# Optimization experiments

Measured on AMD Instinct MI355X. Metric: run time of the kernel, lower is better.

The kernel has to match this reference:

```python
import jax, jax.numpy as jnp
import numpy as np

OUT_FEATURES = 4096
IN_FEATURES = 4096
SCALE_EPS = 1e-5


def setup_inputs() -> dict:
    key = jax.random.key(0)
    k1, k2, k3 = jax.random.split(key, 3)
    x = jax.random.normal(k1, (8192, IN_FEATURES), dtype=jnp.float32)
    # packed int4 weights: two signed nibbles per byte-equivalent int
    weight_packed = jax.random.randint(k2, (OUT_FEATURES, IN_FEATURES // 2), 0, 256, dtype=jnp.int32)
    weight_scale = jax.random.uniform(k3, (OUT_FEATURES,), dtype=jnp.float32) * 0.01 + 1e-4
    return {"x": x, "weight_packed": weight_packed, "weight_scale": weight_scale}


def _unpack_int4(weight_packed):
    # low nibble first, then high nibble, sign-extended from 4 bits
    low = weight_packed & 15
    high = (weight_packed >> 4) & 15
    low = jnp.where(low > 7, low - 16, low)
    high = jnp.where(high > 7, high - 16, high)
    # interleave -> [out_features, in_features]
    w_q = jnp.stack([low, high], axis=-1).reshape(weight_packed.shape[0], -1)
    return w_q


def reference(x, weight_packed, weight_scale):
    # per-row activation quantization to int4 range [-8, 7]
    x_max = jnp.max(jnp.abs(x), axis=-1, keepdims=True)
    x_scale = jnp.maximum(x_max / 7.0, SCALE_EPS)          # [tokens, 1]
    x_q = jnp.clip(jnp.round(x / x_scale), -8.0, 7.0)      # float carrier of int4 values

    w_q = _unpack_int4(weight_packed).astype(jnp.float32)  # [out, in]

    out = jnp.einsum('ti,oi->to', x_q, w_q)                # [tokens, out]
    out = out * (x_scale * weight_scale[None, :])
    return out.astype(x.dtype)
```

## Files before the change

### kernel.cpp

```cpp
#include <hip/hip_runtime.h>

#define SCALE_EPS 1e-5f

typedef int v4i __attribute__((ext_vector_type(4)));

static __device__ __forceinline__ void gll16(const void* g, void* l) {
  __builtin_amdgcn_global_load_lds(
      (const __attribute__((address_space(1))) unsigned int*)g,
      (__attribute__((address_space(3))) unsigned int*)l,
      16, 0, 0);
}

__global__ __launch_bounds__(256) void unpack_w(const int* __restrict__ wp,
                                                char* __restrict__ wq) {
  const int kc = blockIdx.x;
  const int nt = blockIdx.y;
  const int tid = threadIdx.x;
  char* tile = wq + ((size_t)nt * 64 + kc) * 8192;
  const int n0 = nt * 128;
#pragma unroll
  for (int j = 0; j < 4; ++j) {
    int u = j * 256 + tid;
    int r = u >> 3;
    int p = u & 7;
    const v4i* src = (const v4i*)((const char*)wp + (size_t)(n0 + r) * 8192 + kc * 128 + p * 16);
    v4i v = *src;
    unsigned int b[8];
#pragma unroll
    for (int q = 0; q < 4; ++q) {
      int lo = ((v[q] & 15) ^ 8) - 8;
      int hi = (((v[q] >> 4) & 15) ^ 8) - 8;
      b[q * 2]     = (unsigned int)(lo & 255);
      b[q * 2 + 1] = (unsigned int)(hi & 255);
    }
    unsigned int w0 = b[0] | (b[1] << 8) | (b[2] << 16) | (b[3] << 24);
    unsigned int w1 = b[4] | (b[5] << 8) | (b[6] << 16) | (b[7] << 24);
    *(uint2*)(tile + (r >> 4) * 1024 + (p >> 1) * 256 + (r & 15) * 16 + (p & 1) * 8) =
        make_uint2(w0, w1);
  }
}

__global__ __launch_bounds__(256) void quant_x(const float* __restrict__ x,
                                               char* __restrict__ xq,
                                               float* __restrict__ xs) {
  __shared__ float lmax[4][4];
  const int tid = threadIdx.x;
  const int w = tid >> 6;
  const int l = tid & 63;
  const int t0 = blockIdx.x * 4;
  const int row = l >> 4;
  const int t = t0 + row;
  const int sub = l & 15;

  const float* base = x + (size_t)t * 4096 + w * 1024 + sub * 4;
  float4 vals[16];
  float m = 0.0f;
#pragma unroll
  for (int s = 0; s < 16; ++s) {
    vals[s] = *(const float4*)(base + s * 64);
    m = fmaxf(m, fmaxf(fmaxf(fabsf(vals[s].x), fabsf(vals[s].y)),
                       fmaxf(fabsf(vals[s].z), fabsf(vals[s].w))));
  }
#pragma unroll
  for (int d = 1; d < 16; d <<= 1) m = fmaxf(m, __shfl_xor(m, d, 64));
  if (sub == 0) lmax[w][row] = m;
  __syncthreads();
  float rm = fmaxf(fmaxf(lmax[0][row], lmax[1][row]),
                   fmaxf(lmax[2][row], lmax[3][row]));
  float scale = fmaxf(rm / 7.0f, SCALE_EPS);
  if (w == 0 && sub == 0) xs[t] = scale;

  const int mt = t0 >> 7;
  const int f = (t0 & 127) >> 4;
  const int r16 = t & 15;
  const int cc = sub >> 2;
  const int b4 = (sub & 3) * 4;

#pragma unroll
  for (int s = 0; s < 16; ++s) {
    float4 v = vals[s];
    int q0 = (int)fminf(fmaxf(rintf(v.x / scale), -8.0f), 7.0f);
    int q1 = (int)fminf(fmaxf(rintf(v.y / scale), -8.0f), 7.0f);
    int q2 = (int)fminf(fmaxf(rintf(v.z / scale), -8.0f), 7.0f);
    int q3 = (int)fminf(fmaxf(rintf(v.w / scale), -8.0f), 7.0f);
    unsigned int wd = (unsigned int)(q0 & 255) | ((unsigned int)(q1 & 255) << 8) |
                      ((unsigned int)(q2 & 255) << 16) | ((unsigned int)(q3 & 255) << 24);
    *(unsigned int*)(xq + ((size_t)mt * 64 + w * 16 + s) * 8192 +
                     f * 1024 + cc * 256 + r16 * 16 + b4) = wd;
  }
}

__global__ __launch_bounds__(256) void gemm_i8(const char* __restrict__ xq,
                                               const char* __restrict__ wq,
                                               const float* __restrict__ xs,
                                               const float* __restrict__ wsc,
                                               float* __restrict__ out) {
  __shared__ char As[8192];
  __shared__ char Bs[8192];
  const int tid = threadIdx.x;
  const int w = tid >> 6;
  const int lane = tid & 63;
  const int wm = w >> 1, wn = w & 1;
  const int bx = blockIdx.x;
  const int by = blockIdx.y;

  v4i acc[4][4];
  const v4i vzero = {0, 0, 0, 0};
#pragma unroll
  for (int i = 0; i < 4; ++i)
#pragma unroll
    for (int j = 0; j < 4; ++j) acc[i][j] = vzero;

  const char* Abase = xq + (size_t)by * 64 * 8192;
  const char* Bbase = wq + (size_t)bx * 64 * 8192;
  const int c0 = w * 2048 + lane * 16;

  for (int kt = 0; kt < 64; ++kt) {
    const char* At = Abase + kt * 8192;
    const char* Bt = Bbase + kt * 8192;
    gll16(At + c0, As + c0);
    gll16(At + c0 + 1024, As + c0 + 1024);
    gll16(Bt + c0, Bs + c0);
    gll16(Bt + c0 + 1024, Bs + c0 + 1024);
    __syncthreads();
    v4i a[4], b[4];
#pragma unroll
    for (int mi = 0; mi < 4; ++mi)
      a[mi] = *(const v4i*)(As + (wm * 4 + mi) * 1024 + lane * 16);
#pragma unroll
    for (int ni = 0; ni < 4; ++ni)
      b[ni] = *(const v4i*)(Bs + (wn * 4 + ni) * 1024 + lane * 16);
#pragma unroll
    for (int mi = 0; mi < 4; ++mi)
#pragma unroll
      for (int ni = 0; ni < 4; ++ni)
        acc[mi][ni] = __builtin_amdgcn_mfma_i32_16x16x64_i8(a[mi], b[ni], acc[mi][ni], 0, 0, 0);
    __syncthreads();
  }

  float wv[4];
#pragma unroll
  for (int ni = 0; ni < 4; ++ni)
    wv[ni] = wsc[bx * 128 + wn * 64 + ni * 16 + (lane & 15)];
  const int rbase = by * 128 + wm * 64 + ((lane >> 4) << 2);
  const int cbase = bx * 128 + wn * 64 + (lane & 15);
#pragma unroll
  for (int mi = 0; mi < 4; ++mi) {
#pragma unroll
    for (int j = 0; j < 4; ++j) {
      int t = rbase + mi * 16 + j;
      float xsv = xs[t];
      float* orow = out + (size_t)t * 4096 + cbase;
#pragma unroll
      for (int ni = 0; ni < 4; ++ni)
        orow[ni * 16] = (float)acc[mi][ni][j] * (xsv * wv[ni]);
    }
  }
}

extern "C" void kernel_launch(void* const* d_in, const int* in_sizes, int n_in,
                              void* d_out, int out_size, void* d_ws, size_t ws_size,
                              hipStream_t stream) {
  const float* x = (const float*)d_in[0];
  const int* wp = (const int*)d_in[1];
  const float* wsc = (const float*)d_in[2];
  float* out = (float*)d_out;
  char* ws = (char*)d_ws;

  char* xq = ws;
  char* wq = ws + 33554432;
  float* xs = (float*)(ws + 33554432 + 16777216);

  hipLaunchKernelGGL(unpack_w, dim3(64, 32), dim3(256), 0, stream, wp, wq);
  hipLaunchKernelGGL(quant_x, dim3(2048), dim3(256), 0, stream, x, xq, xs);
  hipLaunchKernelGGL(gemm_i8, dim3(32, 64), dim3(256), 0, stream, xq, wq, xs, wsc, out);
}
```

Baseline: 192.1 us.

## Enlarge GEMM tile to 256x256 with 4-stage async LDS pipeline and grid swizzle

The int8 GEMM kernel now uses 512-thread blocks computing 256x256 output tiles, where before it used 128x128. A 4-deep ring of LDS buffers is filled with asynchronous global-to-LDS loads issued three tiles ahead, and explicit vmcnt/lgkmcnt waits replace the full __syncthreads. MFMA phases are split into two halves with setprio, and block IDs are swizzled so co-scheduled blocks share A/B rows for L2 reuse. The goal is to hide global load latency and raise arithmetic intensity. In exchange it uses 128KB of LDS per block, which limits occupancy, and the hand-placed waitcnt logic is fragile.

```diff
diff --git a/kernel.cpp b/kernel.cpp
--- a/kernel.cpp
+++ b/kernel.cpp
@@ -90,62 +90,98 @@
   }
 }
 
-__global__ __launch_bounds__(256) void gemm_i8(const char* __restrict__ xq,
-                                               const char* __restrict__ wq,
-                                               const float* __restrict__ xs,
-                                               const float* __restrict__ wsc,
-                                               float* __restrict__ out) {
-  __shared__ char As[8192];
-  __shared__ char Bs[8192];
+__global__ __launch_bounds__(512, 2) void gemm_i8(const char* __restrict__ xq,
+                                                  const char* __restrict__ wq,
+                                                  const float* __restrict__ xs,
+                                                  const float* __restrict__ wsc,
+                                                  float* __restrict__ out) {
+  __shared__ char lds[4][32768];
   const int tid = threadIdx.x;
-  const int w = tid >> 6;
+  const int wid = tid >> 6;
   const int lane = tid & 63;
-  const int wm = w >> 1, wn = w & 1;
-  const int bx = blockIdx.x;
-  const int by = blockIdx.y;
-
-  v4i acc[4][4];
-  const v4i vzero = {0, 0, 0, 0};
-#pragma unroll
-  for (int i = 0; i < 4; ++i)
-#pragma unroll
-    for (int j = 0; j < 4; ++j) acc[i][j] = vzero;
-
-  const char* Abase = xq + (size_t)by * 64 * 8192;
-  const char* Bbase = wq + (size_t)bx * 64 * 8192;
-  const int c0 = w * 2048 + lane * 16;
-
-  for (int kt = 0; kt < 64; ++kt) {
-    const char* At = Abase + kt * 8192;
-    const char* Bt = Bbase + kt * 8192;
-    gll16(At + c0, As + c0);
-    gll16(At + c0 + 1024, As + c0 + 1024);
-    gll16(Bt + c0, Bs + c0);
-    gll16(Bt + c0 + 1024, Bs + c0 + 1024);
-    __syncthreads();
+  const int wm = wid >> 2;
+  const int wn = wid & 3;
+
+  const int bid = blockIdx.x;
+  const int wg = (bid & 7) * 64 + (bid >> 3);
+  const int by = wg >> 4;
+  const int bx = wg & 15;
+
+  const char* Asrc0 = xq + (size_t)(2 * by) * 64 * 8192;
+  const char* Asrc1 = Asrc0 + 64 * 8192;
+  const char* Bsrc0 = wq + (size_t)(2 * bx) * 64 * 8192;
+  const char* Bsrc1 = Bsrc0 + 64 * 8192;
+  const int toff = tid * 16;
+
+  v4i acc[8][4] = {};
+
+#define STAGE(kt, p)                                                              \
+  gll16(((p) == 0 ? Asrc0 : (p) == 1 ? Asrc1 : (p) == 2 ? Bsrc0 : Bsrc1) +        \
+            (kt) * 8192 + toff,                                                    \
+        lds[(kt) & 3] + (p) * 8192 + toff)
+
+  for (int t = 0; t < 3; ++t) {
+    STAGE(t, 0); STAGE(t, 1); STAGE(t, 2); STAGE(t, 3);
+  }
+  asm volatile("s_waitcnt vmcnt(8)" ::: "memory");
+  __builtin_amdgcn_s_barrier();
+
+  auto tile_step = [&](int kt, bool stage, int vm) {
+    const char* As = lds[kt & 3];
+    const char* Bs = lds[kt & 3] + 16384;
     v4i a[4], b[4];
 #pragma unroll
     for (int mi = 0; mi < 4; ++mi)
-      a[mi] = *(const v4i*)(As + (wm * 4 + mi) * 1024 + lane * 16);
+      a[mi] = *(const v4i*)(As + (wm * 8 + mi) * 1024 + lane * 16);
 #pragma unroll
     for (int ni = 0; ni < 4; ++ni)
       b[ni] = *(const v4i*)(Bs + (wn * 4 + ni) * 1024 + lane * 16);
+    if (stage) { STAGE(kt + 3, 0); STAGE(kt + 3, 1); }
+    __builtin_amdgcn_s_barrier();
+    asm volatile("s_waitcnt lgkmcnt(0)" ::: "memory");
+    __builtin_amdgcn_sched_barrier(0);
+    __builtin_amdgcn_s_setprio(1);
 #pragma unroll
     for (int mi = 0; mi < 4; ++mi)
 #pragma unroll
       for (int ni = 0; ni < 4; ++ni)
         acc[mi][ni] = __builtin_amdgcn_mfma_i32_16x16x64_i8(a[mi], b[ni], acc[mi][ni], 0, 0, 0);
-    __syncthreads();
-  }
-
-  float wv[4];
+    __builtin_amdgcn_s_setprio(0);
+    __builtin_amdgcn_s_barrier();
+#pragma unroll
+    for (int mi = 0; mi < 4; ++mi)
+      a[mi] = *(const v4i*)(As + (wm * 8 + 4 + mi) * 1024 + lane * 16);
+    if (stage) { STAGE(kt + 3, 2); STAGE(kt + 3, 3); }
+    if (vm == 8)      asm volatile("s_waitcnt vmcnt(8)" ::: "memory");
+    else if (vm == 4) asm volatile("s_waitcnt vmcnt(4)" ::: "memory");
+    else if (vm == 0) asm volatile("s_waitcnt vmcnt(0)" ::: "memory");
+    __builtin_amdgcn_s_barrier();
+    asm volatile("s_waitcnt lgkmcnt(0)" ::: "memory");
+    __builtin_amdgcn_sched_barrier(0);
+    __builtin_amdgcn_s_setprio(1);
+#pragma unroll
+    for (int mi = 0; mi < 4; ++mi)
+#pragma unroll
+      for (int ni = 0; ni < 4; ++ni)
+        acc[4 + mi][ni] = __builtin_amdgcn_mfma_i32_16x16x64_i8(a[mi], b[ni], acc[4 + mi][ni], 0, 0, 0);
+    __builtin_amdgcn_s_setprio(0);
+    __builtin_amdgcn_s_barrier();
+  };
+
+  for (int kt = 0; kt < 61; ++kt) tile_step(kt, true, 8);
+  tile_step(61, false, 4);
+  tile_step(62, false, 0);
+  tile_step(63, false, -1);
+#undef STAGE
+
+  float wvv[4];
 #pragma unroll
   for (int ni = 0; ni < 4; ++ni)
-    wv[ni] = wsc[bx * 128 + wn * 64 + ni * 16 + (lane & 15)];
-  const int rbase = by * 128 + wm * 64 + ((lane >> 4) << 2);
-  const int cbase = bx * 128 + wn * 64 + (lane & 15);
-#pragma unroll
-  for (int mi = 0; mi < 4; ++mi) {
+    wvv[ni] = wsc[bx * 256 + wn * 64 + ni * 16 + (lane & 15)];
+  const int rbase = by * 256 + wm * 128 + ((lane >> 4) << 2);
+  const int cbase = bx * 256 + wn * 64 + (lane & 15);
+#pragma unroll
+  for (int mi = 0; mi < 8; ++mi) {
 #pragma unroll
     for (int j = 0; j < 4; ++j) {
       int t = rbase + mi * 16 + j;
@@ -153,7 +189,7 @@
       float* orow = out + (size_t)t * 4096 + cbase;
 #pragma unroll
       for (int ni = 0; ni < 4; ++ni)
-        orow[ni * 16] = (float)acc[mi][ni][j] * (xsv * wv[ni]);
+        orow[ni * 16] = (float)acc[mi][ni][j] * (xsv * wvv[ni]);
     }
   }
 }
@@ -173,5 +209,5 @@
 
   hipLaunchKernelGGL(unpack_w, dim3(64, 32), dim3(256), 0, stream, wp, wq);
   hipLaunchKernelGGL(quant_x, dim3(2048), dim3(256), 0, stream, x, xq, xs);
-  hipLaunchKernelGGL(gemm_i8, dim3(32, 64), dim3(256), 0, stream, xq, wq, xs, wsc, out);
-}
+  hipLaunchKernelGGL(gemm_i8, dim3(512), dim3(512), 0, stream, xq, wq, xs, wsc, out);
+}
```

Result: faster. 182.3 us (-5.1%).
